# Kernel tuning notes

Measured on AMD Instinct MI355X. Metric: run time of the kernel, lower is better.

Reference implementation:

```python
import jax, jax.numpy as jnp
import numpy as np

B, T, Hs, Ws, D, NH, NKV = 2, 8, 16, 16, 1024, 16, 4
HD = D // NH  # 64
EPS = 1e-6
THETA = 10000.0


def setup_inputs() -> dict:
    key = jax.random.key(0)
    ks = jax.random.split(key, 6)
    N = T * Hs * Ws
    s = 0.02
    return {
        'x': jax.random.normal(ks[0], (B, N, D), jnp.float32),
        'Wq': jax.random.normal(ks[1], (D, D), jnp.float32) * s,
        'bq': jnp.zeros((D,), jnp.float32),
        'Wk': jax.random.normal(ks[2], (D, NKV * HD), jnp.float32) * s,
        'bk': jnp.zeros((NKV * HD,), jnp.float32),
        'Wv': jax.random.normal(ks[3], (D, NKV * HD), jnp.float32) * s,
        'bv': jnp.zeros((NKV * HD,), jnp.float32),
        'Wo': jax.random.normal(ks[4], (D, D), jnp.float32) * s,
        'bo': jnp.zeros((D,), jnp.float32),
        'qn_w': jnp.ones((HD,), jnp.float32),
        'kn_w': jnp.ones((HD,), jnp.float32),
        't': T, 'h': Hs, 'w': Ws,
    }


def _rms_norm(x, w):
    # RMSNorm over last dim (head_dim), eps=1e-6, learned scale
    var = jnp.mean(jnp.square(x), axis=-1, keepdims=True)
    return x * jax.lax.rsqrt(var + EPS) * w


def _rope_cs(n, d):
    inv = 1.0 / (THETA ** (np.arange(0, d, 2, dtype=np.float32) / d))
    fr = np.arange(n, dtype=np.float32)[:, None] * inv[None, :]
    emb = np.concatenate([fr, fr], axis=-1)  # (n, d)
    return jnp.asarray(np.cos(emb)), jnp.asarray(np.sin(emb))


def _rot_half(x):
    x1, x2 = jnp.split(x, 2, axis=-1)
    return jnp.concatenate([-x2, x1], axis=-1)


def _st_rope(x, t, h, w):
    # x: (B, t, h, w, heads, hd); factored 3D RoPE on head_dim split
    d = x.shape[-1]
    if d % 3 == 0:
        dt = dh = d // 3
        dw = d - 2 * dt
    else:
        dt = d // 4
        dh = d // 4
        dw = d - dt - dh
    xt, xh, xw = jnp.split(x, [dt, dt + dh], axis=-1)

    def app(xs, n, axis_pos, dd):
        cos, sin = _rope_cs(n, dd)
        shp = [1] * 6
        shp[axis_pos] = n
        shp[-1] = dd
        cos = cos.reshape(shp)
        sin = sin.reshape(shp)
        return xs * cos + _rot_half(xs) * sin

    xt = app(xt, t, 1, dt)
    xh = app(xh, h, 2, dh)
    xw = app(xw, w, 3, dw)
    return jnp.concatenate([xt, xh, xw], axis=-1)


def reference(x, Wq, bq, Wk, bk, Wv, bv, Wo, bo, qn_w, kn_w, t, h, w):
    Bx, N, Dx = x.shape
    q = (x @ Wq + bq).reshape(Bx, N, NH, HD)
    k = (x @ Wk + bk).reshape(Bx, N, NKV, HD)
    v = (x @ Wv + bv).reshape(Bx, N, NKV, HD)
    q = _rms_norm(q, qn_w)
    k = _rms_norm(k, kn_w)
    q = _st_rope(q.reshape(Bx, t, h, w, NH, HD), t, h, w).reshape(Bx, N, NH, HD)
    k = _st_rope(k.reshape(Bx, t, h, w, NKV, HD), t, h, w).reshape(Bx, N, NKV, HD)
    g = NH // NKV
    if g > 1:  # GQA: 'b m h d -> b m (h g) d'
        k = jnp.repeat(k, g, axis=2)
        v = jnp.repeat(v, g, axis=2)
    scale = HD ** -0.5
    scores = jnp.einsum('bnhd,bmhd->bhnm', q, k) * scale  # (B,H,N,N)
    p = jax.nn.softmax(scores, axis=-1)
    out = jnp.einsum('bhnm,bmhd->bnhd', p, v).reshape(Bx, N, Dx)
    return out @ Wo + bo
```

## Files before the change

### kernel.cpp

```cpp
#include <hip/hip_runtime.h>
#include <hip/hip_bf16.h>
#include <math.h>

constexpr int B_   = 2;
constexpr int N_   = 2048;
constexpr int D_   = 1024;
constexpr int NH_  = 16;
constexpr int NKV_ = 4;
constexpr int HD_  = 64;
constexpr int BN_  = 4096;
constexpr int KVD_ = NKV_ * HD_;
constexpr float EPS_ = 1e-6f;
constexpr float THETA_ = 10000.0f;
constexpr float LOG2E_ = 1.4426950408889634f;

typedef _Float16 half8v __attribute__((ext_vector_type(8)));
typedef _Float16 half4v __attribute__((ext_vector_type(4)));
typedef _Float16 half2v __attribute__((ext_vector_type(2)));
typedef unsigned short ushort8v __attribute__((ext_vector_type(8)));
typedef float f32x4 __attribute__((ext_vector_type(4)));

static __device__ __forceinline__ unsigned short f2h(float f) {
  union { _Float16 h; unsigned short u; } v; v.h = (_Float16)f; return v.u;
}
static __device__ __forceinline__ float h2f(unsigned short u) {
  union { unsigned short u; _Float16 h; } v; v.u = u; return (float)v.h;
}

#if __has_builtin(__builtin_amdgcn_exp2f)
#define EXP2F(x) __builtin_amdgcn_exp2f(x)
#else
#define EXP2F(x) __expf((x) * 0.6931471805599453f)
#endif

static __device__ __forceinline__ void dma16(const unsigned short* g,
                                             unsigned short* l) {
  __builtin_amdgcn_global_load_lds(
      (const __attribute__((address_space(1))) unsigned int*)g,
      (__attribute__((address_space(3))) unsigned int*)l, 16, 0, 0);
}

static __device__ __forceinline__ void wtrans_tile(
    const float* __restrict__ W, int Nw, int K, float scale,
    unsigned short* __restrict__ WTh, unsigned short* __restrict__ WTl,
    int bx, int by, bool lo)
{
  __shared__ float tile[32][33];
  const int k0 = bx * 32, n0 = by * 32;
  const int c = threadIdx.x & 31, rb = threadIdx.x >> 5;
#pragma unroll
  for (int i = 0; i < 4; ++i) {
    const int r = rb + i * 8;
    tile[r][c] = W[(size_t)(k0 + r) * Nw + n0 + c];
  }
  __syncthreads();
#pragma unroll
  for (int i = 0; i < 4; ++i) {
    const int r = rb + i * 8;
    const float v = tile[c][r] * scale;
    const size_t o = (size_t)(n0 + r) * K + k0 + c;
    const unsigned short hi = f2h(v);
    WTh[o] = hi;
    if (lo) WTl[o] = f2h(v - h2f(hi));
  }
}

__global__ __launch_bounds__(256) void prep(
    const float* __restrict__ x,
    const float* __restrict__ Wq, const float* __restrict__ Wk,
    const float* __restrict__ Wv, const float* __restrict__ Wo,
    unsigned short* __restrict__ xh,
    unsigned short* __restrict__ WqT, unsigned short* __restrict__ WkT,
    unsigned short* __restrict__ WvT,
    unsigned short* __restrict__ WoTh, unsigned short* __restrict__ WoTl)
{
  const int bid = blockIdx.x;
  if (bid < 2048) {
    const int i = (bid * 256 + threadIdx.x) * 8;
    const float4 v0 = *(const float4*)(x + i);
    const float4 v1 = *(const float4*)(x + i + 4);
    ushort8v o;
    o[0] = f2h(v0.x); o[1] = f2h(v0.y); o[2] = f2h(v0.z); o[3] = f2h(v0.w);
    o[4] = f2h(v1.x); o[5] = f2h(v1.y); o[6] = f2h(v1.z); o[7] = f2h(v1.w);
    *(ushort8v*)(xh + i) = o;
  } else if (bid < 3072) {
    const int l = bid - 2048;
    wtrans_tile(Wq, D_, D_, 1.0f, WqT, nullptr, l & 31, l >> 5, false);
  } else if (bid < 3328) {
    const int l = bid - 3072;
    wtrans_tile(Wk, KVD_, D_, 1.0f, WkT, nullptr, l & 31, l >> 5, false);
  } else if (bid < 3584) {
    const int l = bid - 3328;
    wtrans_tile(Wv, KVD_, D_, 1.0f, WvT, nullptr, l & 31, l >> 5, false);
  } else {
    const int l = bid - 3584;
    wtrans_tile(Wo, D_, D_, 64.0f, WoTh, WoTl, l & 31, l >> 5, true);
  }
}

__global__ __launch_bounds__(256) void gemm_qkv(
    const unsigned short* __restrict__ xh,
    const unsigned short* __restrict__ WqT, const unsigned short* __restrict__ WkT,
    const unsigned short* __restrict__ WvT,
    const float* __restrict__ bq, const float* __restrict__ bk, const float* __restrict__ bv,
    const float* __restrict__ qn, const float* __restrict__ kn,
    unsigned short* __restrict__ qv, unsigned short* __restrict__ kv,
    unsigned short* __restrict__ vv)
{
  __shared__ unsigned short As[128 * 64];
  __shared__ unsigned short Bs[64 * 64];

  const int y = blockIdx.y;
  const unsigned short* wt; const float* bias; unsigned short* outp; int opitch, col0, mode;
  if (y < 16)      { wt = WqT + (size_t)y * 64 * D_;        bias = bq + y * 64;        outp = qv; opitch = D_;   col0 = y * 64;        mode = 0; }
  else if (y < 20) { wt = WkT + (size_t)(y - 16) * 64 * D_; bias = bk + (y - 16) * 64; outp = kv; opitch = KVD_; col0 = (y - 16) * 64; mode = 1; }
  else             { wt = WvT + (size_t)(y - 20) * 64 * D_; bias = bv + (y - 20) * 64; outp = vv; opitch = KVD_; col0 = (y - 20) * 64; mode = 2; }

  const int bm = blockIdx.x * 128;
  const int tid = threadIdx.x;
  const int w = tid >> 6, lane = tid & 63, quad = lane >> 4, l16 = lane & 15;
  const int lr = lane >> 3;
  const int gc = (lane & 7) ^ lr;
  const int sw = l16 & 7;

  const unsigned short* gA = xh + (size_t)(bm + w * 8 + lr) * D_ + gc * 8;
  const unsigned short* gB = wt + (size_t)(w * 8 + lr) * D_ + gc * 8;

  f32x4 acc[2][4];
#pragma unroll
  for (int i = 0; i < 2; ++i)
#pragma unroll
    for (int j = 0; j < 4; ++j) acc[i][j] = (f32x4){0.f, 0.f, 0.f, 0.f};

  for (int k0 = 0; k0 < D_; k0 += 64) {
    __syncthreads();
#pragma unroll
    for (int rd = 0; rd < 4; ++rd)
      dma16(gA + (size_t)rd * 32 * D_ + k0, &As[rd * 2048 + w * 512]);
#pragma unroll
    for (int rd = 0; rd < 2; ++rd)
      dma16(gB + (size_t)rd * 32 * D_ + k0, &Bs[rd * 2048 + w * 512]);
    __syncthreads();

#pragma unroll
    for (int kk = 0; kk < 2; ++kk) {
      half8v fa[2], fb[4];
#pragma unroll
      for (int mb = 0; mb < 2; ++mb)
        fa[mb] = *(const half8v*)&As[(w * 32 + mb * 16 + l16) * 64 + ((kk * 4 + quad) ^ sw) * 8];
#pragma unroll
      for (int nb = 0; nb < 4; ++nb)
        fb[nb] = *(const half8v*)&Bs[(nb * 16 + l16) * 64 + ((kk * 4 + quad) ^ sw) * 8];
#pragma unroll
      for (int mb = 0; mb < 2; ++mb)
#pragma unroll
        for (int nb = 0; nb < 4; ++nb)
          acc[mb][nb] = __builtin_amdgcn_mfma_f32_16x16x32_f16(fa[mb], fb[nb], acc[mb][nb], 0, 0, 0);
    }
  }

  float bsv[4];
#pragma unroll
  for (int nb = 0; nb < 4; ++nb) bsv[nb] = bias[nb * 16 + l16];

  if (mode == 2) {
#pragma unroll
    for (int mb = 0; mb < 2; ++mb)
#pragma unroll
      for (int nb = 0; nb < 4; ++nb)
#pragma unroll
        for (int r = 0; r < 4; ++r) {
          const int row = bm + w * 32 + mb * 16 + quad * 4 + r;
          outp[(size_t)row * opitch + col0 + nb * 16 + l16] = f2h(acc[mb][nb][r] + bsv[nb]);
        }
    return;
  }

  const float* nwp = (mode == 0) ? qn : kn;
  float wv[4];
#pragma unroll
  for (int nb = 0; nb < 4; ++nb) wv[nb] = nwp[nb * 16 + l16];
  const float f_th = __powf(THETA_, -(float)(l16 & 7) / 8.0f);
  const float f_w  = __powf(THETA_, -(float)l16 / 16.0f);
  const float oscale = (mode == 0) ? 0.125f * LOG2E_ : 1.0f;
  const bool first8 = (l16 & 8) == 0;

  float snw[4], csw[4];
#pragma unroll
  for (int r = 0; r < 4; ++r)
    __sincosf((float)(quad * 4 + r) * f_w, &snw[r], &csw[r]);

#pragma unroll
  for (int mb = 0; mb < 2; ++mb) {
    const int nbase = (bm + w * 32 + mb * 16) & (N_ - 1);
    float snt, cst, snh, csh;
    __sincosf((float)(nbase >> 8) * f_th, &snt, &cst);
    __sincosf((float)((nbase >> 4) & 15) * f_th, &snh, &csh);
#pragma unroll
    for (int r = 0; r < 4; ++r) {
      float v[4];
      float ss = 0.f;
#pragma unroll
      for (int nb = 0; nb < 4; ++nb) { v[nb] = acc[mb][nb][r] + bsv[nb]; ss += v[nb] * v[nb]; }
      ss += __shfl_xor(ss, 1, 64);
      ss += __shfl_xor(ss, 2, 64);
      ss += __shfl_xor(ss, 4, 64);
      ss += __shfl_xor(ss, 8, 64);
      const float rs = rsqrtf(ss * (1.0f / 64.0f) + EPS_);
#pragma unroll
      for (int nb = 0; nb < 4; ++nb) v[nb] *= rs * wv[nb];

      const float p0 = __shfl_xor(v[0], 8, 64);
      const float p1 = __shfl_xor(v[1], 8, 64);
      const float o0 = v[0] * cst + (first8 ? -p0 : p0) * snt;
      const float o1 = v[1] * csh + (first8 ? -p1 : p1) * snh;
      const float o2 = v[2] * csw[r] - v[3] * snw[r];
      const float o3 = v[3] * csw[r] + v[2] * snw[r];

      const int row = bm + w * 32 + mb * 16 + quad * 4 + r;
      const size_t ob = (size_t)row * opitch + col0 + l16;
      outp[ob]      = f2h(o0 * oscale);
      outp[ob + 16] = f2h(o1 * oscale);
      outp[ob + 32] = f2h(o2 * oscale);
      outp[ob + 48] = f2h(o3 * oscale);
    }
  }
}

__global__ __launch_bounds__(256) void gemm_o(
    const unsigned short* __restrict__ ag,
    const unsigned short* __restrict__ WTh, const unsigned short* __restrict__ WTl,
    const float* __restrict__ bo, float* __restrict__ out)
{
  __shared__ unsigned short As[128 * 64];
  __shared__ unsigned short Bh[64 * 64], Bl[64 * 64];

  const int bm = blockIdx.x * 128, bn = blockIdx.y * 64;
  const int tid = threadIdx.x;
  const int w = tid >> 6, lane = tid & 63, quad = lane >> 4, l16 = lane & 15;
  const int lr = lane >> 3;
  const int gc = (lane & 7) ^ lr;
  const int sw = l16 & 7;

  const unsigned short* gA  = ag  + (size_t)(bm + w * 8 + lr) * D_ + gc * 8;
  const unsigned short* gBh = WTh + (size_t)(bn + w * 8 + lr) * D_ + gc * 8;
  const unsigned short* gBl = WTl + (size_t)(bn + w * 8 + lr) * D_ + gc * 8;

  f32x4 acc[2][4];
#pragma unroll
  for (int i = 0; i < 2; ++i)
#pragma unroll
    for (int j = 0; j < 4; ++j) acc[i][j] = (f32x4){0.f, 0.f, 0.f, 0.f};

  for (int k0 = 0; k0 < D_; k0 += 64) {
    __syncthreads();
#pragma unroll
    for (int rd = 0; rd < 4; ++rd)
      dma16(gA + (size_t)rd * 32 * D_ + k0, &As[rd * 2048 + w * 512]);
#pragma unroll
    for (int rd = 0; rd < 2; ++rd) {
      dma16(gBh + (size_t)rd * 32 * D_ + k0, &Bh[rd * 2048 + w * 512]);
      dma16(gBl + (size_t)rd * 32 * D_ + k0, &Bl[rd * 2048 + w * 512]);
    }
    __syncthreads();

#pragma unroll
    for (int kk = 0; kk < 2; ++kk) {
      half8v fa[2], fbh[4], fbl[4];
#pragma unroll
      for (int mb = 0; mb < 2; ++mb)
        fa[mb] = *(const half8v*)&As[(w * 32 + mb * 16 + l16) * 64 + ((kk * 4 + quad) ^ sw) * 8];
#pragma unroll
      for (int nb = 0; nb < 4; ++nb) {
        const int ro = (nb * 16 + l16) * 64 + ((kk * 4 + quad) ^ sw) * 8;
        fbh[nb] = *(const half8v*)&Bh[ro];
        fbl[nb] = *(const half8v*)&Bl[ro];
      }
#pragma unroll
      for (int mb = 0; mb < 2; ++mb)
#pragma unroll
        for (int nb = 0; nb < 4; ++nb) {
          acc[mb][nb] = __builtin_amdgcn_mfma_f32_16x16x32_f16(fa[mb], fbl[nb], acc[mb][nb], 0, 0, 0);
          acc[mb][nb] = __builtin_amdgcn_mfma_f32_16x16x32_f16(fa[mb], fbh[nb], acc[mb][nb], 0, 0, 0);
        }
    }
  }

  float bsv[4];
#pragma unroll
  for (int nb = 0; nb < 4; ++nb) bsv[nb] = bo[bn + nb * 16 + l16];
#pragma unroll
  for (int mb = 0; mb < 2; ++mb)
#pragma unroll
    for (int nb = 0; nb < 4; ++nb)
#pragma unroll
      for (int r = 0; r < 4; ++r) {
        const int row = bm + w * 32 + mb * 16 + quad * 4 + r;
        const int col = bn + nb * 16 + l16;
        out[(size_t)row * D_ + col] = acc[mb][nb][r] * 0.015625f + bsv[nb];
      }
}

__global__ __launch_bounds__(512, 2) void attn_mfma(
    const unsigned short* __restrict__ qg,
    const unsigned short* __restrict__ kg,
    const unsigned short* __restrict__ vg,
    unsigned short* __restrict__ og)
{
  __shared__ unsigned short Ks[2][128 * 64];
  __shared__ unsigned short Vt[2][64][136];

  const int bid = blockIdx.x;
  const int qt  = bid & 7;
  const int h   = (bid >> 3) & 15;
  const int b   = bid >> 7;
  const int kvh = h >> 2;

  const int tid  = threadIdx.x;
  const int w    = tid >> 6;
  const int lane = tid & 63;
  const int quad = lane >> 4;
  const int l16  = lane & 15;
  const int lr = lane >> 3;
  const int gc = (lane & 7) ^ lr;
  const int sw = l16 & 7;

  half8v aq[2][2];
#pragma unroll
  for (int qb = 0; qb < 2; ++qb) {
    const int qrow = qt * 256 + w * 32 + qb * 16 + l16;
    const unsigned short* qptr =
        qg + ((size_t)(b * N_ + qrow) * D_) + h * HD_ + quad * 8;
    aq[qb][0] = *(const half8v*)(qptr);
    aq[qb][1] = *(const half8v*)(qptr + 32);
  }

  f32x4 o_[2][4];
  float lrow[2] = {0.f, 0.f};
#pragma unroll
  for (int qb = 0; qb < 2; ++qb)
#pragma unroll
    for (int i = 0; i < 4; ++i) o_[qb][i] = (f32x4){0.f, 0.f, 0.f, 0.f};

  const unsigned short* gK =
      kg + ((size_t)(b * N_) + w * 8 + lr) * KVD_ + kvh * HD_ + gc * 8;

  const int vj  = tid & 15;
  const int vh  = (tid >> 4) & 1;
  const int vs  = (tid >> 5) & 7;
  const int vhh = tid >> 8;
  const int vcol = vhh * 64 + vh * 32 +
                   ((vj >> 1) & 3) * 8 + ((vj >> 3) & 1) * 4 + 2 * (vj & 1);
  const unsigned short* gV =
      vg + (size_t)(b * N_ + vhh * 64 + 2 * vj + 32 * vh) * KVD_ + kvh * HD_ + 8 * vs;

#pragma unroll
  for (int rd = 0; rd < 2; ++rd)
    dma16(gK + (size_t)(rd * 64) * KVD_, &Ks[0][rd * 4096 + w * 512]);
  ushort8v va0 = *(const ushort8v*)(gV);
  ushort8v va1 = *(const ushort8v*)(gV + KVD_);
#pragma unroll
  for (int i = 0; i < 8; ++i)
    *(unsigned int*)&Vt[0][8 * vs + i][vcol] =
        (unsigned int)va0[i] | ((unsigned int)va1[i] << 16);
  {
    const unsigned short* p = gV + (size_t)128 * KVD_;
    va0 = *(const ushort8v*)(p);
    va1 = *(const ushort8v*)(p + KVD_);
  }
  __syncthreads();

  for (int kt = 0; kt < 16; ++kt) {
    const int cur = kt & 1;
    if (kt < 15) {
#pragma unroll
      for (int rd = 0; rd < 2; ++rd)
        dma16(gK + (size_t)((kt + 1) * 128 + rd * 64) * KVD_,
              &Ks[cur ^ 1][rd * 4096 + w * 512]);
#pragma unroll
      for (int i = 0; i < 8; ++i)
        *(unsigned int*)&Vt[cur ^ 1][8 * vs + i][vcol] =
            (unsigned int)va0[i] | ((unsigned int)va1[i] << 16);
      if (kt < 14) {
        const unsigned short* p = gV + (size_t)(kt + 2) * 128 * KVD_;
        va0 = *(const ushort8v*)(p);
        va1 = *(const ushort8v*)(p + KVD_);
      }
    }

#pragma unroll
    for (int hh = 0; hh < 2; ++hh) {
      f32x4 s[2][4];
#pragma unroll
      for (int nb = 0; nb < 4; ++nb) {
        const int kr = (hh * 64 + nb * 16 + l16) * 64;
        const half8v b0 = *(const half8v*)&Ks[cur][kr + (quad ^ sw) * 8];
        const half8v b1 = *(const half8v*)&Ks[cur][kr + ((4 + quad) ^ sw) * 8];
#pragma unroll
        for (int qb = 0; qb < 2; ++qb) {
          f32x4 z = (f32x4){0.f, 0.f, 0.f, 0.f};
          z = __builtin_amdgcn_mfma_f32_16x16x32_f16(b0, aq[qb][0], z, 0, 0, 0);
          s[qb][nb] = __builtin_amdgcn_mfma_f32_16x16x32_f16(b1, aq[qb][1], z, 0, 0, 0);
        }
      }

      half8v pf[2][2];
#pragma unroll
      for (int qb = 0; qb < 2; ++qb) {
        float ls = 0.f;
#pragma unroll
        for (int nb = 0; nb < 4; ++nb) {
          const float p0 = EXP2F(s[qb][nb][0]);
          const float p1 = EXP2F(s[qb][nb][1]);
          const float p2 = EXP2F(s[qb][nb][2]);
          const float p3 = EXP2F(s[qb][nb][3]);
          ls += (p0 + p1) + (p2 + p3);
          const int kc = nb >> 1, jo = (nb & 1) * 4;
          pf[qb][kc][jo + 0] = (_Float16)p0;
          pf[qb][kc][jo + 1] = (_Float16)p1;
          pf[qb][kc][jo + 2] = (_Float16)p2;
          pf[qb][kc][jo + 3] = (_Float16)p3;
        }
        lrow[qb] += ls;
      }

#pragma unroll
      for (int kc = 0; kc < 2; ++kc)
#pragma unroll
        for (int nb = 0; nb < 4; ++nb) {
          const half8v bv =
              *(const half8v*)&Vt[cur][nb * 16 + l16][hh * 64 + kc * 32 + quad * 8];
#pragma unroll
          for (int qb = 0; qb < 2; ++qb)
            o_[qb][nb] = __builtin_amdgcn_mfma_f32_16x16x32_f16(bv, pf[qb][kc], o_[qb][nb], 0, 0, 0);
        }
    }
    __syncthreads();
  }

#pragma unroll
  for (int qb = 0; qb < 2; ++qb) {
    float l = lrow[qb];
    l += __shfl_xor(l, 16, 64);
    l += __shfl_xor(l, 32, 64);
    const float inv = 1.0f / l;
    const int qrow = qt * 256 + w * 32 + qb * 16 + l16;
    const size_t base = (size_t)(b * N_ + qrow) * D_ + h * HD_;
#pragma unroll
    for (int nb = 0; nb < 4; ++nb) {
      half4v pk;
#pragma unroll
      for (int r = 0; r < 4; ++r) pk[r] = (_Float16)(o_[qb][nb][r] * inv);
      *(half4v*)&og[base + nb * 16 + quad * 4] = pk;
    }
  }
}

extern "C" void kernel_launch(void* const* d_in, const int* in_sizes, int n_in,
                              void* d_out, int out_size, void* d_ws, size_t ws_size,
                              hipStream_t stream) {
  const float* x  = (const float*)d_in[0];
  const float* Wq = (const float*)d_in[1];
  const float* bq = (const float*)d_in[2];
  const float* Wk = (const float*)d_in[3];
  const float* bk = (const float*)d_in[4];
  const float* Wv = (const float*)d_in[5];
  const float* bv = (const float*)d_in[6];
  const float* Wo = (const float*)d_in[7];
  const float* bo = (const float*)d_in[8];
  const float* qn = (const float*)d_in[9];
  const float* kn = (const float*)d_in[10];
  float* out = (float*)d_out;

  const size_t M4 = (size_t)BN_ * D_;
  const size_t M1 = (size_t)BN_ * KVD_;
  unsigned short* xh  = (unsigned short*)d_ws;
  unsigned short* qv  = xh + M4;
  unsigned short* kv  = qv + M4;
  unsigned short* vv  = kv + M1;
  unsigned short* WqT = vv + M1;
  unsigned short* WkT = WqT + (size_t)D_ * D_;
  unsigned short* WvT = WkT + (size_t)D_ * KVD_;
  unsigned short* WoTh = WvT + (size_t)D_ * KVD_;
  unsigned short* WoTl = WoTh + (size_t)D_ * D_;
  unsigned short* og  = xh;

  const dim3 blk(256);

  prep<<<dim3(4608), blk, 0, stream>>>(x, Wq, Wk, Wv, Wo, xh, WqT, WkT, WvT, WoTh, WoTl);

  gemm_qkv<<<dim3(32, 24), blk, 0, stream>>>(xh, WqT, WkT, WvT, bq, bk, bv, qn, kn, qv, kv, vv);

  attn_mfma<<<dim3(B_ * NH_ * (N_ / 256)), dim3(512), 0, stream>>>(qv, kv, vv, og);

  gemm_o<<<dim3(32, 16), blk, 0, stream>>>(og, WoTh, WoTl, bo, out);
}
```

Baseline: 174.9 us.

## Double-buffer LDS in QKV and output GEMMs, retile output GEMM to 256x64

```diff
diff --git a/kernel.cpp b/kernel.cpp
--- a/kernel.cpp
+++ b/kernel.cpp
@@ -107,8 +107,8 @@
     unsigned short* __restrict__ qv, unsigned short* __restrict__ kv,
     unsigned short* __restrict__ vv)
 {
-  __shared__ unsigned short As[128 * 64];
-  __shared__ unsigned short Bs[64 * 64];
+  __shared__ unsigned short As[2][128 * 64];
+  __shared__ unsigned short Bs[2][64 * 64];
 
   const int y = blockIdx.y;
   const unsigned short* wt; const float* bias; unsigned short* outp; int opitch, col0, mode;
@@ -132,31 +132,43 @@
 #pragma unroll
     for (int j = 0; j < 4; ++j) acc[i][j] = (f32x4){0.f, 0.f, 0.f, 0.f};
 
-  for (int k0 = 0; k0 < D_; k0 += 64) {
-    __syncthreads();
-#pragma unroll
-    for (int rd = 0; rd < 4; ++rd)
-      dma16(gA + (size_t)rd * 32 * D_ + k0, &As[rd * 2048 + w * 512]);
-#pragma unroll
-    for (int rd = 0; rd < 2; ++rd)
-      dma16(gB + (size_t)rd * 32 * D_ + k0, &Bs[rd * 2048 + w * 512]);
-    __syncthreads();
+#pragma unroll
+  for (int rd = 0; rd < 4; ++rd)
+    dma16(gA + (size_t)rd * 32 * D_, &As[0][rd * 2048 + w * 512]);
+#pragma unroll
+  for (int rd = 0; rd < 2; ++rd)
+    dma16(gB + (size_t)rd * 32 * D_, &Bs[0][rd * 2048 + w * 512]);
+  __syncthreads();
+
+  for (int ks = 0; ks < 16; ++ks) {
+    const int cur = ks & 1;
+    if (ks < 15) {
+      const int k1 = (ks + 1) * 64;
+#pragma unroll
+      for (int rd = 0; rd < 4; ++rd)
+        dma16(gA + (size_t)rd * 32 * D_ + k1, &As[cur ^ 1][rd * 2048 + w * 512]);
+#pragma unroll
+      for (int rd = 0; rd < 2; ++rd)
+        dma16(gB + (size_t)rd * 32 * D_ + k1, &Bs[cur ^ 1][rd * 2048 + w * 512]);
+    }
 
 #pragma unroll
     for (int kk = 0; kk < 2; ++kk) {
       half8v fa[2], fb[4];
+      const int slot = ((kk * 4 + quad) ^ sw) * 8;
 #pragma unroll
       for (int mb = 0; mb < 2; ++mb)
-        fa[mb] = *(const half8v*)&As[(w * 32 + mb * 16 + l16) * 64 + ((kk * 4 + quad) ^ sw) * 8];
+        fa[mb] = *(const half8v*)&As[cur][(w * 32 + mb * 16 + l16) * 64 + slot];
 #pragma unroll
       for (int nb = 0; nb < 4; ++nb)
-        fb[nb] = *(const half8v*)&Bs[(nb * 16 + l16) * 64 + ((kk * 4 + quad) ^ sw) * 8];
+        fb[nb] = *(const half8v*)&Bs[cur][(nb * 16 + l16) * 64 + slot];
 #pragma unroll
       for (int mb = 0; mb < 2; ++mb)
 #pragma unroll
         for (int nb = 0; nb < 4; ++nb)
           acc[mb][nb] = __builtin_amdgcn_mfma_f32_16x16x32_f16(fa[mb], fb[nb], acc[mb][nb], 0, 0, 0);
     }
+    __syncthreads();
   }
 
   float bsv[4];
@@ -227,17 +239,18 @@
   }
 }
 
-__global__ __launch_bounds__(256) void gemm_o(
+__global__ __launch_bounds__(512, 2) void gemm_o(
     const unsigned short* __restrict__ ag,
     const unsigned short* __restrict__ WTh, const unsigned short* __restrict__ WTl,
     const float* __restrict__ bo, float* __restrict__ out)
 {
-  __shared__ unsigned short As[128 * 64];
-  __shared__ unsigned short Bh[64 * 64], Bl[64 * 64];
-
-  const int bm = blockIdx.x * 128, bn = blockIdx.y * 64;
+  __shared__ unsigned short As[2][256 * 64];
+  __shared__ unsigned short Bh[2][64 * 64], Bl[2][64 * 64];
+
+  const int bm = blockIdx.x * 256, bn = blockIdx.y * 64;
   const int tid = threadIdx.x;
   const int w = tid >> 6, lane = tid & 63, quad = lane >> 4, l16 = lane & 15;
+  const int wr = w >> 1, wc = w & 1;
   const int lr = lane >> 3;
   const int gc = (lane & 7) ^ lr;
   const int sw = l16 & 7;
@@ -246,57 +259,65 @@
   const unsigned short* gBh = WTh + (size_t)(bn + w * 8 + lr) * D_ + gc * 8;
   const unsigned short* gBl = WTl + (size_t)(bn + w * 8 + lr) * D_ + gc * 8;
 
-  f32x4 acc[2][4];
-#pragma unroll
-  for (int i = 0; i < 2; ++i)
-#pragma unroll
-    for (int j = 0; j < 4; ++j) acc[i][j] = (f32x4){0.f, 0.f, 0.f, 0.f};
-
-  for (int k0 = 0; k0 < D_; k0 += 64) {
-    __syncthreads();
-#pragma unroll
-    for (int rd = 0; rd < 4; ++rd)
-      dma16(gA + (size_t)rd * 32 * D_ + k0, &As[rd * 2048 + w * 512]);
-#pragma unroll
-    for (int rd = 0; rd < 2; ++rd) {
-      dma16(gBh + (size_t)rd * 32 * D_ + k0, &Bh[rd * 2048 + w * 512]);
-      dma16(gBl + (size_t)rd * 32 * D_ + k0, &Bl[rd * 2048 + w * 512]);
-    }
-    __syncthreads();
+  f32x4 acc[4][2];
+#pragma unroll
+  for (int i = 0; i < 4; ++i)
+#pragma unroll
+    for (int j = 0; j < 2; ++j) acc[i][j] = (f32x4){0.f, 0.f, 0.f, 0.f};
+
+#pragma unroll
+  for (int rd = 0; rd < 4; ++rd)
+    dma16(gA + (size_t)rd * 64 * D_, &As[0][rd * 4096 + w * 512]);
+  dma16(gBh, &Bh[0][w * 512]);
+  dma16(gBl, &Bl[0][w * 512]);
+  __syncthreads();
+
+  for (int ks = 0; ks < 16; ++ks) {
+    const int cur = ks & 1;
+    if (ks < 15) {
+      const int k1 = (ks + 1) * 64;
+#pragma unroll
+      for (int rd = 0; rd < 4; ++rd)
+        dma16(gA + (size_t)rd * 64 * D_ + k1, &As[cur ^ 1][rd * 4096 + w * 512]);
+      dma16(gBh + k1, &Bh[cur ^ 1][w * 512]);
+      dma16(gBl + k1, &Bl[cur ^ 1][w * 512]);
+    }
 
 #pragma unroll
     for (int kk = 0; kk < 2; ++kk) {
-      half8v fa[2], fbh[4], fbl[4];
-#pragma unroll
-      for (int mb = 0; mb < 2; ++mb)
-        fa[mb] = *(const half8v*)&As[(w * 32 + mb * 16 + l16) * 64 + ((kk * 4 + quad) ^ sw) * 8];
-#pragma unroll
-      for (int nb = 0; nb < 4; ++nb) {
-        const int ro = (nb * 16 + l16) * 64 + ((kk * 4 + quad) ^ sw) * 8;
-        fbh[nb] = *(const half8v*)&Bh[ro];
-        fbl[nb] = *(const half8v*)&Bl[ro];
+      half8v fa[4], fbh[2], fbl[2];
+      const int slot = ((kk * 4 + quad) ^ sw) * 8;
+#pragma unroll
+      for (int mb = 0; mb < 4; ++mb)
+        fa[mb] = *(const half8v*)&As[cur][(wr * 64 + mb * 16 + l16) * 64 + slot];
+#pragma unroll
+      for (int nb = 0; nb < 2; ++nb) {
+        const int ro = (wc * 32 + nb * 16 + l16) * 64 + slot;
+        fbh[nb] = *(const half8v*)&Bh[cur][ro];
+        fbl[nb] = *(const half8v*)&Bl[cur][ro];
       }
 #pragma unroll
-      for (int mb = 0; mb < 2; ++mb)
-#pragma unroll
-        for (int nb = 0; nb < 4; ++nb) {
+      for (int mb = 0; mb < 4; ++mb)
+#pragma unroll
+        for (int nb = 0; nb < 2; ++nb) {
           acc[mb][nb] = __builtin_amdgcn_mfma_f32_16x16x32_f16(fa[mb], fbl[nb], acc[mb][nb], 0, 0, 0);
           acc[mb][nb] = __builtin_amdgcn_mfma_f32_16x16x32_f16(fa[mb], fbh[nb], acc[mb][nb], 0, 0, 0);
         }
     }
-  }
-
-  float bsv[4];
-#pragma unroll
-  for (int nb = 0; nb < 4; ++nb) bsv[nb] = bo[bn + nb * 16 + l16];
-#pragma unroll
-  for (int mb = 0; mb < 2; ++mb)
-#pragma unroll
-    for (int nb = 0; nb < 4; ++nb)
+    __syncthreads();
+  }
+
+  float bsv[2];
+#pragma unroll
+  for (int nb = 0; nb < 2; ++nb) bsv[nb] = bo[bn + wc * 32 + nb * 16 + l16];
+#pragma unroll
+  for (int mb = 0; mb < 4; ++mb)
+#pragma unroll
+    for (int nb = 0; nb < 2; ++nb)
 #pragma unroll
       for (int r = 0; r < 4; ++r) {
-        const int row = bm + w * 32 + mb * 16 + quad * 4 + r;
-        const int col = bn + nb * 16 + l16;
+        const int row = bm + wr * 64 + mb * 16 + quad * 4 + r;
+        const int col = bn + wc * 32 + nb * 16 + l16;
         out[(size_t)row * D_ + col] = acc[mb][nb][r] * 0.015625f + bsv[nb];
       }
 }
@@ -493,5 +514,5 @@
 
   attn_mfma<<<dim3(B_ * NH_ * (N_ / 256)), dim3(512), 0, stream>>>(qv, kv, vv, og);
 
-  gemm_o<<<dim3(32, 16), blk, 0, stream>>>(og, WoTh, WoTl, bo, out);
-}
+  gemm_o<<<dim3(16, 16), dim3(512), 0, stream>>>(og, WoTh, WoTl, bo, out);
+}
```

After: 179.0 us. +2.3%, slower.

## Split attention over key dimension into two partitions with a combine kernel

Applied to the files above, without the earlier changes.

```diff
diff --git a/kernel.cpp b/kernel.cpp
--- a/kernel.cpp
+++ b/kernel.cpp
@@ -16,7 +16,6 @@
 
 typedef _Float16 half8v __attribute__((ext_vector_type(8)));
 typedef _Float16 half4v __attribute__((ext_vector_type(4)));
-typedef _Float16 half2v __attribute__((ext_vector_type(2)));
 typedef unsigned short ushort8v __attribute__((ext_vector_type(8)));
 typedef float f32x4 __attribute__((ext_vector_type(4)));
 
@@ -301,19 +300,21 @@
       }
 }
 
-__global__ __launch_bounds__(512, 2) void attn_mfma(
+__global__ __launch_bounds__(256, 3) void attn_mfma(
     const unsigned short* __restrict__ qg,
     const unsigned short* __restrict__ kg,
     const unsigned short* __restrict__ vg,
-    unsigned short* __restrict__ og)
+    unsigned short* __restrict__ po,
+    float* __restrict__ pl)
 {
-  __shared__ unsigned short Ks[2][128 * 64];
-  __shared__ unsigned short Vt[2][64][136];
+  __shared__ unsigned short Ks[2][64 * 64];
+  __shared__ unsigned short Vt[2][64][64];
 
   const int bid = blockIdx.x;
-  const int qt  = bid & 7;
-  const int h   = (bid >> 3) & 15;
-  const int b   = bid >> 7;
+  const int qt  = bid & 15;
+  const int h   = (bid >> 4) & 15;
+  const int b   = (bid >> 8) & 1;
+  const int ks  = bid >> 9;
   const int kvh = h >> 2;
 
   const int tid  = threadIdx.x;
@@ -328,7 +329,7 @@
   half8v aq[2][2];
 #pragma unroll
   for (int qb = 0; qb < 2; ++qb) {
-    const int qrow = qt * 256 + w * 32 + qb * 16 + l16;
+    const int qrow = qt * 128 + w * 32 + qb * 16 + l16;
     const unsigned short* qptr =
         qg + ((size_t)(b * N_ + qrow) * D_) + h * HD_ + quad * 8;
     aq[qb][0] = *(const half8v*)(qptr);
@@ -343,28 +344,26 @@
     for (int i = 0; i < 4; ++i) o_[qb][i] = (f32x4){0.f, 0.f, 0.f, 0.f};
 
   const unsigned short* gK =
-      kg + ((size_t)(b * N_) + w * 8 + lr) * KVD_ + kvh * HD_ + gc * 8;
-
-  const int vj  = tid & 15;
-  const int vh  = (tid >> 4) & 1;
-  const int vs  = (tid >> 5) & 7;
-  const int vhh = tid >> 8;
-  const int vcol = vhh * 64 + vh * 32 +
-                   ((vj >> 1) & 3) * 8 + ((vj >> 3) & 1) * 4 + 2 * (vj & 1);
+      kg + ((size_t)(b * N_ + ks * 1024) + w * 8 + lr) * KVD_ + kvh * HD_ + gc * 8;
+
+  const int vp = tid & 31;
+  const int vs = tid >> 5;
+  const int vchunk  = ((vp >> 4) & 1) * 4 + ((vp >> 1) & 3);
+  const int vwithin = ((vp >> 3) & 1) * 4 + (vp & 1) * 2;
   const unsigned short* gV =
-      vg + (size_t)(b * N_ + vhh * 64 + 2 * vj + 32 * vh) * KVD_ + kvh * HD_ + 8 * vs;
+      vg + (size_t)(b * N_ + ks * 1024 + 2 * vp) * KVD_ + kvh * HD_ + 8 * vs;
 
 #pragma unroll
   for (int rd = 0; rd < 2; ++rd)
-    dma16(gK + (size_t)(rd * 64) * KVD_, &Ks[0][rd * 4096 + w * 512]);
+    dma16(gK + (size_t)(rd * 32) * KVD_, &Ks[0][rd * 2048 + w * 512]);
   ushort8v va0 = *(const ushort8v*)(gV);
   ushort8v va1 = *(const ushort8v*)(gV + KVD_);
 #pragma unroll
   for (int i = 0; i < 8; ++i)
-    *(unsigned int*)&Vt[0][8 * vs + i][vcol] =
+    *(unsigned int*)&Vt[0][8 * vs + i][((vchunk ^ i) << 3) + vwithin] =
         (unsigned int)va0[i] | ((unsigned int)va1[i] << 16);
   {
-    const unsigned short* p = gV + (size_t)128 * KVD_;
+    const unsigned short* p = gV + (size_t)64 * KVD_;
     va0 = *(const ushort8v*)(p);
     va1 = *(const ushort8v*)(p + KVD_);
   }
@@ -375,66 +374,67 @@
     if (kt < 15) {
 #pragma unroll
       for (int rd = 0; rd < 2; ++rd)
-        dma16(gK + (size_t)((kt + 1) * 128 + rd * 64) * KVD_,
-              &Ks[cur ^ 1][rd * 4096 + w * 512]);
+        dma16(gK + (size_t)((kt + 1) * 64 + rd * 32) * KVD_,
+              &Ks[cur ^ 1][rd * 2048 + w * 512]);
 #pragma unroll
       for (int i = 0; i < 8; ++i)
-        *(unsigned int*)&Vt[cur ^ 1][8 * vs + i][vcol] =
+        *(unsigned int*)&Vt[cur ^ 1][8 * vs + i][((vchunk ^ i) << 3) + vwithin] =
             (unsigned int)va0[i] | ((unsigned int)va1[i] << 16);
       if (kt < 14) {
-        const unsigned short* p = gV + (size_t)(kt + 2) * 128 * KVD_;
+        const unsigned short* p = gV + (size_t)(kt + 2) * 64 * KVD_;
         va0 = *(const ushort8v*)(p);
         va1 = *(const ushort8v*)(p + KVD_);
       }
     }
 
-#pragma unroll
-    for (int hh = 0; hh < 2; ++hh) {
-      f32x4 s[2][4];
+    f32x4 s[2][4];
+    __builtin_amdgcn_s_setprio(1);
+#pragma unroll
+    for (int nb = 0; nb < 4; ++nb) {
+      const int kr = (nb * 16 + l16) * 64;
+      const half8v b0 = *(const half8v*)&Ks[cur][kr + (quad ^ sw) * 8];
+      const half8v b1 = *(const half8v*)&Ks[cur][kr + ((4 + quad) ^ sw) * 8];
+#pragma unroll
+      for (int qb = 0; qb < 2; ++qb) {
+        f32x4 z = (f32x4){0.f, 0.f, 0.f, 0.f};
+        z = __builtin_amdgcn_mfma_f32_16x16x32_f16(b0, aq[qb][0], z, 0, 0, 0);
+        s[qb][nb] = __builtin_amdgcn_mfma_f32_16x16x32_f16(b1, aq[qb][1], z, 0, 0, 0);
+      }
+    }
+    __builtin_amdgcn_s_setprio(0);
+
+    half8v pf[2][2];
+#pragma unroll
+    for (int qb = 0; qb < 2; ++qb) {
+      float ls = 0.f;
 #pragma unroll
       for (int nb = 0; nb < 4; ++nb) {
-        const int kr = (hh * 64 + nb * 16 + l16) * 64;
-        const half8v b0 = *(const half8v*)&Ks[cur][kr + (quad ^ sw) * 8];
-        const half8v b1 = *(const half8v*)&Ks[cur][kr + ((4 + quad) ^ sw) * 8];
-#pragma unroll
-        for (int qb = 0; qb < 2; ++qb) {
-          f32x4 z = (f32x4){0.f, 0.f, 0.f, 0.f};
-          z = __builtin_amdgcn_mfma_f32_16x16x32_f16(b0, aq[qb][0], z, 0, 0, 0);
-          s[qb][nb] = __builtin_amdgcn_mfma_f32_16x16x32_f16(b1, aq[qb][1], z, 0, 0, 0);
-        }
+        const float p0 = EXP2F(s[qb][nb][0]);
+        const float p1 = EXP2F(s[qb][nb][1]);
+        const float p2 = EXP2F(s[qb][nb][2]);
+        const float p3 = EXP2F(s[qb][nb][3]);
+        ls += (p0 + p1) + (p2 + p3);
+        const int kc = nb >> 1, jo = (nb & 1) * 4;
+        pf[qb][kc][jo + 0] = (_Float16)p0;
+        pf[qb][kc][jo + 1] = (_Float16)p1;
+        pf[qb][kc][jo + 2] = (_Float16)p2;
+        pf[qb][kc][jo + 3] = (_Float16)p3;
       }
-
-      half8v pf[2][2];
-#pragma unroll
-      for (int qb = 0; qb < 2; ++qb) {
-        float ls = 0.f;
-#pragma unroll
-        for (int nb = 0; nb < 4; ++nb) {
-          const float p0 = EXP2F(s[qb][nb][0]);
-          const float p1 = EXP2F(s[qb][nb][1]);
-          const float p2 = EXP2F(s[qb][nb][2]);
-          const float p3 = EXP2F(s[qb][nb][3]);
-          ls += (p0 + p1) + (p2 + p3);
-          const int kc = nb >> 1, jo = (nb & 1) * 4;
-          pf[qb][kc][jo + 0] = (_Float16)p0;
-          pf[qb][kc][jo + 1] = (_Float16)p1;
-          pf[qb][kc][jo + 2] = (_Float16)p2;
-          pf[qb][kc][jo + 3] = (_Float16)p3;
-        }
-        lrow[qb] += ls;
+      lrow[qb] += ls;
+    }
+
+    __builtin_amdgcn_s_setprio(1);
+#pragma unroll
+    for (int kc = 0; kc < 2; ++kc)
+#pragma unroll
+      for (int nb = 0; nb < 4; ++nb) {
+        const half8v bv =
+            *(const half8v*)&Vt[cur][nb * 16 + l16][((kc * 4 + quad) ^ sw) * 8];
+#pragma unroll
+        for (int qb = 0; qb < 2; ++qb)
+          o_[qb][nb] = __builtin_amdgcn_mfma_f32_16x16x32_f16(bv, pf[qb][kc], o_[qb][nb], 0, 0, 0);
       }
-
-#pragma unroll
-      for (int kc = 0; kc < 2; ++kc)
-#pragma unroll
-        for (int nb = 0; nb < 4; ++nb) {
-          const half8v bv =
-              *(const half8v*)&Vt[cur][nb * 16 + l16][hh * 64 + kc * 32 + quad * 8];
-#pragma unroll
-          for (int qb = 0; qb < 2; ++qb)
-            o_[qb][nb] = __builtin_amdgcn_mfma_f32_16x16x32_f16(bv, pf[qb][kc], o_[qb][nb], 0, 0, 0);
-        }
-    }
+    __builtin_amdgcn_s_setprio(0);
     __syncthreads();
   }
 
@@ -444,16 +444,39 @@
     l += __shfl_xor(l, 16, 64);
     l += __shfl_xor(l, 32, 64);
     const float inv = 1.0f / l;
-    const int qrow = qt * 256 + w * 32 + qb * 16 + l16;
-    const size_t base = (size_t)(b * N_ + qrow) * D_ + h * HD_;
+    const int qrow = qt * 128 + w * 32 + qb * 16 + l16;
+    const size_t rowg = (size_t)(b * N_ + qrow);
+    if (quad == 0) pl[((size_t)ks * 4096 + rowg) * 16 + h] = l;
+    const size_t base = ((size_t)ks * 4096 + rowg) * D_ + h * HD_;
 #pragma unroll
     for (int nb = 0; nb < 4; ++nb) {
       half4v pk;
 #pragma unroll
       for (int r = 0; r < 4; ++r) pk[r] = (_Float16)(o_[qb][nb][r] * inv);
-      *(half4v*)&og[base + nb * 16 + quad * 4] = pk;
-    }
-  }
+      *(half4v*)&po[base + nb * 16 + quad * 4] = pk;
+    }
+  }
+}
+
+__global__ __launch_bounds__(256) void combine(
+    const unsigned short* __restrict__ po, const float* __restrict__ pl,
+    unsigned short* __restrict__ og)
+{
+  const int idx = blockIdx.x * 256 + threadIdx.x;
+  const int e = idx * 8;
+  const int row = e >> 10;
+  const int h = (e >> 6) & 15;
+  const float l0 = pl[(size_t)row * 16 + h];
+  const float l1 = pl[(size_t)(4096 + row) * 16 + h];
+  const float inv = 1.0f / (l0 + l1);
+  const float w0 = l0 * inv, w1 = l1 * inv;
+  const ushort8v a = *(const ushort8v*)(po + e);
+  const ushort8v c = *(const ushort8v*)(po + (size_t)4096 * 1024 + e);
+  ushort8v o;
+#pragma unroll
+  for (int i = 0; i < 8; ++i)
+    o[i] = f2h(h2f(a[i]) * w0 + h2f(c[i]) * w1);
+  *(ushort8v*)(og + e) = o;
 }
 
 extern "C" void kernel_launch(void* const* d_in, const int* in_sizes, int n_in,
@@ -483,6 +506,8 @@
   unsigned short* WvT = WkT + (size_t)D_ * KVD_;
   unsigned short* WoTh = WvT + (size_t)D_ * KVD_;
   unsigned short* WoTl = WoTh + (size_t)D_ * D_;
+  unsigned short* pov  = WoTl + (size_t)D_ * D_;
+  float* plv = (float*)(pov + (size_t)2 * 4096 * 1024);
   unsigned short* og  = xh;
 
   const dim3 blk(256);
@@ -491,7 +516,9 @@
 
   gemm_qkv<<<dim3(32, 24), blk, 0, stream>>>(xh, WqT, WkT, WvT, bq, bk, bv, qn, kn, qv, kv, vv);
 
-  attn_mfma<<<dim3(B_ * NH_ * (N_ / 256)), dim3(512), 0, stream>>>(qv, kv, vv, og);
+  attn_mfma<<<dim3(1024), blk, 0, stream>>>(qv, kv, vv, pov, plv);
+
+  combine<<<dim3(2048), blk, 0, stream>>>(pov, plv, og);
 
   gemm_o<<<dim3(32, 16), blk, 0, stream>>>(og, WoTh, WoTl, bo, out);
 }
```

New measurement: 192.6 us. 10.1% more time.

## Double-buffer LDS tiles in QKV and output GEMMs to overlap loads with MFMA

Applied to the files above, without the earlier changes.

```diff
diff --git a/kernel.cpp b/kernel.cpp
--- a/kernel.cpp
+++ b/kernel.cpp
@@ -16,7 +16,6 @@
 
 typedef _Float16 half8v __attribute__((ext_vector_type(8)));
 typedef _Float16 half4v __attribute__((ext_vector_type(4)));
-typedef _Float16 half2v __attribute__((ext_vector_type(2)));
 typedef unsigned short ushort8v __attribute__((ext_vector_type(8)));
 typedef float f32x4 __attribute__((ext_vector_type(4)));
 
@@ -107,8 +106,8 @@
     unsigned short* __restrict__ qv, unsigned short* __restrict__ kv,
     unsigned short* __restrict__ vv)
 {
-  __shared__ unsigned short As[128 * 64];
-  __shared__ unsigned short Bs[64 * 64];
+  __shared__ unsigned short As[2][128 * 64];
+  __shared__ unsigned short Bs[2][64 * 64];
 
   const int y = blockIdx.y;
   const unsigned short* wt; const float* bias; unsigned short* outp; int opitch, col0, mode;
@@ -132,31 +131,48 @@
 #pragma unroll
     for (int j = 0; j < 4; ++j) acc[i][j] = (f32x4){0.f, 0.f, 0.f, 0.f};
 
-  for (int k0 = 0; k0 < D_; k0 += 64) {
-    __syncthreads();
-#pragma unroll
-    for (int rd = 0; rd < 4; ++rd)
-      dma16(gA + (size_t)rd * 32 * D_ + k0, &As[rd * 2048 + w * 512]);
-#pragma unroll
-    for (int rd = 0; rd < 2; ++rd)
-      dma16(gB + (size_t)rd * 32 * D_ + k0, &Bs[rd * 2048 + w * 512]);
-    __syncthreads();
+#pragma unroll
+  for (int rd = 0; rd < 4; ++rd)
+    dma16(gA + (size_t)rd * 32 * D_, &As[0][rd * 2048 + w * 512]);
+#pragma unroll
+  for (int rd = 0; rd < 2; ++rd)
+    dma16(gB + (size_t)rd * 32 * D_, &Bs[0][rd * 2048 + w * 512]);
+  asm volatile("s_waitcnt vmcnt(0)" ::: "memory");
+  __builtin_amdgcn_s_barrier();
+
+  for (int ks = 0; ks < 16; ++ks) {
+    const int cur = ks & 1;
+    if (ks < 15) {
+      const int k1 = (ks + 1) * 64;
+#pragma unroll
+      for (int rd = 0; rd < 4; ++rd)
+        dma16(gA + (size_t)rd * 32 * D_ + k1, &As[cur ^ 1][rd * 2048 + w * 512]);
+#pragma unroll
+      for (int rd = 0; rd < 2; ++rd)
+        dma16(gB + (size_t)rd * 32 * D_ + k1, &Bs[cur ^ 1][rd * 2048 + w * 512]);
+      asm volatile("s_waitcnt vmcnt(6)" ::: "memory");
+    } else {
+      asm volatile("s_waitcnt vmcnt(0)" ::: "memory");
+    }
+    __builtin_amdgcn_s_barrier();
 
 #pragma unroll
     for (int kk = 0; kk < 2; ++kk) {
       half8v fa[2], fb[4];
+      const int slot = ((kk * 4 + quad) ^ sw) * 8;
 #pragma unroll
       for (int mb = 0; mb < 2; ++mb)
-        fa[mb] = *(const half8v*)&As[(w * 32 + mb * 16 + l16) * 64 + ((kk * 4 + quad) ^ sw) * 8];
+        fa[mb] = *(const half8v*)&As[cur][(w * 32 + mb * 16 + l16) * 64 + slot];
 #pragma unroll
       for (int nb = 0; nb < 4; ++nb)
-        fb[nb] = *(const half8v*)&Bs[(nb * 16 + l16) * 64 + ((kk * 4 + quad) ^ sw) * 8];
+        fb[nb] = *(const half8v*)&Bs[cur][(nb * 16 + l16) * 64 + slot];
 #pragma unroll
       for (int mb = 0; mb < 2; ++mb)
 #pragma unroll
         for (int nb = 0; nb < 4; ++nb)
           acc[mb][nb] = __builtin_amdgcn_mfma_f32_16x16x32_f16(fa[mb], fb[nb], acc[mb][nb], 0, 0, 0);
     }
+    __builtin_amdgcn_s_barrier();
   }
 
   float bsv[4];
@@ -232,8 +248,8 @@
     const unsigned short* __restrict__ WTh, const unsigned short* __restrict__ WTl,
     const float* __restrict__ bo, float* __restrict__ out)
 {
-  __shared__ unsigned short As[128 * 64];
-  __shared__ unsigned short Bh[64 * 64], Bl[64 * 64];
+  __shared__ unsigned short As[2][128 * 64];
+  __shared__ unsigned short Bh[2][64 * 64], Bl[2][64 * 64];
 
   const int bm = blockIdx.x * 128, bn = blockIdx.y * 64;
   const int tid = threadIdx.x;
@@ -252,29 +268,47 @@
 #pragma unroll
     for (int j = 0; j < 4; ++j) acc[i][j] = (f32x4){0.f, 0.f, 0.f, 0.f};
 
-  for (int k0 = 0; k0 < D_; k0 += 64) {
-    __syncthreads();
-#pragma unroll
-    for (int rd = 0; rd < 4; ++rd)
-      dma16(gA + (size_t)rd * 32 * D_ + k0, &As[rd * 2048 + w * 512]);
-#pragma unroll
-    for (int rd = 0; rd < 2; ++rd) {
-      dma16(gBh + (size_t)rd * 32 * D_ + k0, &Bh[rd * 2048 + w * 512]);
-      dma16(gBl + (size_t)rd * 32 * D_ + k0, &Bl[rd * 2048 + w * 512]);
-    }
-    __syncthreads();
+#pragma unroll
+  for (int rd = 0; rd < 4; ++rd)
+    dma16(gA + (size_t)rd * 32 * D_, &As[0][rd * 2048 + w * 512]);
+#pragma unroll
+  for (int rd = 0; rd < 2; ++rd) {
+    dma16(gBh + (size_t)rd * 32 * D_, &Bh[0][rd * 2048 + w * 512]);
+    dma16(gBl + (size_t)rd * 32 * D_, &Bl[0][rd * 2048 + w * 512]);
+  }
+  asm volatile("s_waitcnt vmcnt(0)" ::: "memory");
+  __builtin_amdgcn_s_barrier();
+
+  for (int ks = 0; ks < 16; ++ks) {
+    const int cur = ks & 1;
+    if (ks < 15) {
+      const int k1 = (ks + 1) * 64;
+#pragma unroll
+      for (int rd = 0; rd < 4; ++rd)
+        dma16(gA + (size_t)rd * 32 * D_ + k1, &As[cur ^ 1][rd * 2048 + w * 512]);
+#pragma unroll
+      for (int rd = 0; rd < 2; ++rd) {
+        dma16(gBh + (size_t)rd * 32 * D_ + k1, &Bh[cur ^ 1][rd * 2048 + w * 512]);
+        dma16(gBl + (size_t)rd * 32 * D_ + k1, &Bl[cur ^ 1][rd * 2048 + w * 512]);
+      }
+      asm volatile("s_waitcnt vmcnt(8)" ::: "memory");
+    } else {
+      asm volatile("s_waitcnt vmcnt(0)" ::: "memory");
+    }
+    __builtin_amdgcn_s_barrier();
 
 #pragma unroll
     for (int kk = 0; kk < 2; ++kk) {
       half8v fa[2], fbh[4], fbl[4];
+      const int slot = ((kk * 4 + quad) ^ sw) * 8;
 #pragma unroll
       for (int mb = 0; mb < 2; ++mb)
-        fa[mb] = *(const half8v*)&As[(w * 32 + mb * 16 + l16) * 64 + ((kk * 4 + quad) ^ sw) * 8];
+        fa[mb] = *(const half8v*)&As[cur][(w * 32 + mb * 16 + l16) * 64 + slot];
 #pragma unroll
       for (int nb = 0; nb < 4; ++nb) {
-        const int ro = (nb * 16 + l16) * 64 + ((kk * 4 + quad) ^ sw) * 8;
-        fbh[nb] = *(const half8v*)&Bh[ro];
-        fbl[nb] = *(const half8v*)&Bl[ro];
+        const int ro = (nb * 16 + l16) * 64 + slot;
+        fbh[nb] = *(const half8v*)&Bh[cur][ro];
+        fbl[nb] = *(const half8v*)&Bl[cur][ro];
       }
 #pragma unroll
       for (int mb = 0; mb < 2; ++mb)
@@ -284,6 +318,7 @@
           acc[mb][nb] = __builtin_amdgcn_mfma_f32_16x16x32_f16(fa[mb], fbh[nb], acc[mb][nb], 0, 0, 0);
         }
     }
+    __builtin_amdgcn_s_barrier();
   }
 
   float bsv[4];
```

Result: slower. 179.7 us (+2.8%).
